# Performance work log

Hardware: AMD Instinct MI355X
Metric: run time of the kernel (lower is better)

Reference implementation:

```python
import jax, jax.numpy as jnp
import numpy as np
import math

B, D, C_LEN, Q_LEN = 32, 128, 1024, 256
NEG = -1e30

def setup_inputs() -> dict:
    key = jax.random.key(0)
    ks = jax.random.split(key, 8)
    bound = 1.0 / math.sqrt(D)
    return {
        "C": jax.random.normal(ks[0], (B, D, C_LEN), jnp.float32),
        "Q": jax.random.normal(ks[1], (B, D, Q_LEN), jnp.float32),
        "c_mask": jnp.ones((B, C_LEN), jnp.float32),
        "q_mask": jnp.ones((B, Q_LEN), jnp.float32),
        "W0": jax.random.uniform(ks[2], (3 * D,), jnp.float32, -bound, bound),
        # depthwise conv1d: in=4D groups=4D kernel=5 -> weight (4D, 1, 5)
        "dw_w": jax.random.normal(ks[3], (4 * D, 1, 5), jnp.float32) * math.sqrt(2.0 / 5),
        "dw_b": jnp.zeros((4 * D,), jnp.float32),
        # pointwise conv1d: 4D -> D, kernel 1
        "pw_w": jax.random.normal(ks[4], (D, 4 * D, 1), jnp.float32) * math.sqrt(2.0 / (4 * D)),
        "pw_b": jnp.zeros((D,), jnp.float32),
    }

def reference(C, Q, c_mask, q_mask, W0, dw_w, dw_b, pw_w, pw_b):
    d = W0.shape[0] // 3
    C_t = jnp.swapaxes(C, 1, 2)  # (B, c_len, d)
    Q_t = jnp.swapaxes(Q, 1, 2)  # (B, q_len, d)
    w1, w2, w3 = W0[:d], W0[d:2 * d], W0[2 * d:]
    # Trilinear similarity without materializing (B,c,q,3d):
    # S[b,i,j] = C_t[b,i].w1 + Q_t[b,j].w2 + sum_k C_t[b,i,k]*Q_t[b,j,k]*w3[k]
    S = (jnp.einsum('bik,bjk->bij', C_t * w3, Q_t)
         + (C_t @ w1)[:, :, None] + (Q_t @ w2)[:, None, :])  # (B, c_len, q_len)
    q_m = q_mask[:, None, :]
    c_m = c_mask[:, :, None]
    S_bar = jax.nn.softmax(S * q_m + NEG * (1.0 - q_m), axis=2)
    S_bbar = jax.nn.softmax(S * c_m + NEG * (1.0 - c_m), axis=1)
    A = jnp.einsum('bij,bjk->bik', S_bar, Q_t)                       # (B, c_len, d)
    # bmm(S_bar, S_bbar^T) @ C_t  ==  S_bar @ (S_bbar^T @ C_t)
    Bm = jnp.einsum('bij,bjk->bik', S_bar, jnp.einsum('bij,bik->bjk', S_bbar, C_t))
    out = jnp.concatenate([C_t, A, C_t * A, C_t * Bm], axis=2)       # (B, c_len, 4d)
    x = jnp.swapaxes(out, 1, 2)  # (B, 4d, c_len)
    # depthwise separable conv (eval mode: dropout is identity)
    x = jax.lax.conv_general_dilated(x, dw_w, (1,), [(2, 2)],
                                     dimension_numbers=('NCH', 'OIH', 'NCH'),
                                     feature_group_count=x.shape[1]) + dw_b[None, :, None]
    x = jax.lax.conv_general_dilated(x, pw_w, (1,), [(0, 0)],
                                     dimension_numbers=('NCH', 'OIH', 'NCH')) + pw_b[None, :, None]
    return x  # (B, d, c_len)
```

## Files before the change

kernel.cpp:

```cpp
#include <hip/hip_runtime.h>
#include <math.h>

#define NB 32
#define ND 128
#define NC 1024
#define NQ 256
#define NEGV (-1e30f)

typedef __attribute__((ext_vector_type(8))) __bf16 bf16x8;
typedef __attribute__((ext_vector_type(4))) float f32x4;
typedef __attribute__((ext_vector_type(8))) unsigned short u16x8;
typedef __attribute__((ext_vector_type(4))) unsigned short u16x4;

__device__ inline unsigned short f2bf(float f) {
  unsigned u = __builtin_bit_cast(unsigned, f);
  u += 0x7FFFu + ((u >> 16) & 1u);
  return (unsigned short)(u >> 16);
}
__device__ inline float bf2f(unsigned short u) {
  return __builtin_bit_cast(float, (unsigned)u << 16);
}

__global__ __launch_bounds__(256) void k_pwcvt(const float* __restrict__ pwW, unsigned short* __restrict__ pwB16) {
  int idx = blockIdx.x * 256 + threadIdx.x;
  const float4* src = (const float4*)pwW;
  float4 v0 = src[idx * 2], v1 = src[idx * 2 + 1];
  u16x8 o;
  o[0] = f2bf(v0.x); o[1] = f2bf(v0.y); o[2] = f2bf(v0.z); o[3] = f2bf(v0.w);
  o[4] = f2bf(v1.x); o[5] = f2bf(v1.y); o[6] = f2bf(v1.z); o[7] = f2bf(v1.w);
  ((u16x8*)pwB16)[idx] = o;
}

__global__ __launch_bounds__(256) void k_qprep(const float* __restrict__ Q, const float* __restrict__ W0,
                                               unsigned short* __restrict__ qSwz, unsigned short* __restrict__ qT,
                                               float* __restrict__ qb) {
  __shared__ unsigned short T2[128 * 66];
  __shared__ float w2L[128];
  __shared__ float qbP[4][64];
  int b = blockIdx.y, jc = blockIdx.x, j0 = jc * 64, t = threadIdx.x;
  if (t < 128) w2L[t] = W0[ND + t];
  int d = t >> 1, half = t & 1;
  const float* src = Q + ((size_t)b * ND + d) * NQ + j0 + half * 32;
  unsigned short* qdst = qSwz + ((size_t)b * ND + d) * NQ + jc * 64;
  #pragma unroll
  for (int q = 0; q < 4; ++q) {
    float4 v0 = ((const float4*)src)[q * 2];
    float4 v1 = ((const float4*)src)[q * 2 + 1];
    u16x8 o;
    o[0] = f2bf(v0.x); o[1] = f2bf(v0.y); o[2] = f2bf(v0.z); o[3] = f2bf(v0.w);
    o[4] = f2bf(v1.x); o[5] = f2bf(v1.y); o[6] = f2bf(v1.z); o[7] = f2bf(v1.w);
    *(u16x8*)&T2[d * 66 + half * 32 + q * 8] = o;
    int g = half * 4 + q;
    *(u16x8*)&qdst[(g ^ (d & 7)) * 8] = o;
  }
  __syncthreads();
  {
    int jj = t & 63, dq = t >> 6;
    float s = 0.f;
    #pragma unroll 8
    for (int k = 0; k < 32; ++k) {
      int dd = dq * 32 + k;
      s += bf2f(T2[dd * 66 + jj]) * w2L[dd];
    }
    qbP[dq][jj] = s;
  }
  __syncthreads();
  if (t < 64)
    qb[b * NQ + j0 + t] = qbP[0][t] + qbP[1][t] + qbP[2][t] + qbP[3][t];
  {
    int jj = t >> 2, p = t & 3;
    unsigned short* dst = qT + ((size_t)b * NQ + j0 + jj) * ND;
    #pragma unroll
    for (int q = 0; q < 4; ++q) {
      int g = p * 4 + q;
      u16x8 o;
      #pragma unroll
      for (int e = 0; e < 8; ++e) o[e] = T2[(g * 8 + e) * 66 + jj];
      int sg = (g & 8) | ((g & 7) ^ (jj & 7));
      *(u16x8*)&dst[sg * 8] = o;
    }
  }
}

__global__ __launch_bounds__(256) void k_cprep(const float* __restrict__ C, const float* __restrict__ W0,
                                               unsigned short* __restrict__ cw3T, unsigned short* __restrict__ cSwz,
                                               float* __restrict__ cb) {
  __shared__ unsigned short T2[128 * 66];
  __shared__ float w1L[128], w3L[128];
  __shared__ float cbP[4][64];
  int b = blockIdx.y, i0 = blockIdx.x * 64, t = threadIdx.x;
  if (t < 128) { w1L[t] = W0[t]; w3L[t] = W0[2 * ND + t]; }
  int k = t >> 1, half = t & 1;
  const float* src = C + ((size_t)b * ND + k) * NC + i0 + half * 32;
  unsigned short* cdst = cSwz + ((size_t)b * ND + k) * NC + blockIdx.x * 64;
  #pragma unroll
  for (int q = 0; q < 4; ++q) {
    float4 v0 = ((const float4*)src)[q * 2];
    float4 v1 = ((const float4*)src)[q * 2 + 1];
    u16x8 o;
    o[0] = f2bf(v0.x); o[1] = f2bf(v0.y); o[2] = f2bf(v0.z); o[3] = f2bf(v0.w);
    o[4] = f2bf(v1.x); o[5] = f2bf(v1.y); o[6] = f2bf(v1.z); o[7] = f2bf(v1.w);
    *(u16x8*)&T2[k * 66 + half * 32 + q * 8] = o;
    int g = half * 4 + q;
    *(u16x8*)&cdst[(g ^ (k & 7)) * 8] = o;
  }
  __syncthreads();
  {
    int ii = t & 63, kq = t >> 6;
    float s = 0.f;
    #pragma unroll 8
    for (int kk = 0; kk < 32; ++kk) {
      int dd = kq * 32 + kk;
      s += bf2f(T2[dd * 66 + ii]) * w1L[dd];
    }
    cbP[kq][ii] = s;
  }
  __syncthreads();
  if (t < 64)
    cb[b * NC + i0 + t] = cbP[0][t] + cbP[1][t] + cbP[2][t] + cbP[3][t];
  {
    int ii = t >> 2, p = t & 3;
    unsigned short* dst = cw3T + ((size_t)b * NC + i0 + ii) * ND;
    #pragma unroll
    for (int q = 0; q < 4; ++q) {
      int g = p * 4 + q;
      u16x8 o;
      #pragma unroll
      for (int e = 0; e < 8; ++e)
        o[e] = f2bf(bf2f(T2[(g * 8 + e) * 66 + ii]) * w3L[g * 8 + e]);
      int sg = (g & 8) | ((g & 7) ^ (ii & 7));
      *(u16x8*)&dst[sg * 8] = o;
    }
  }
}

__global__ __launch_bounds__(256) void k_stats(const unsigned short* __restrict__ cw3T,
                                               const unsigned short* __restrict__ qT,
                                               const float* __restrict__ cb, const float* __restrict__ qb,
                                               const float* __restrict__ q_mask, const float* __restrict__ c_mask,
                                               float* __restrict__ rowmax, float* __restrict__ rowsum,
                                               float* __restrict__ colPm, float* __restrict__ colPs) {
  __shared__ float rmP[64][4], rsP[64][4];
  __shared__ float cbL[64], cmL[64], qbL[256], qmL[256];
  int b = blockIdx.y, i0 = blockIdx.x * 64;
  int t = threadIdx.x, w = t >> 6, l = t & 63, h = l >> 4, lr = l & 15;
  int wj = w * 64;
  if (t < 64) { cbL[t] = cb[b * NC + i0 + t]; cmL[t] = c_mask[b * NC + i0 + t]; }
  qbL[t] = qb[b * NQ + t];
  qmL[t] = q_mask[b * NQ + t];
  const unsigned short* Arow = cw3T + ((size_t)b * NC + i0) * ND;
  const unsigned short* Brow = qT + (size_t)b * NQ * ND;
  f32x4 acc[4][4] = {};
  #pragma unroll
  for (int ks = 0; ks < 4; ++ks) {
    int g = ks * 4 + h;
    int off = ((g & 8) | ((g & 7) ^ (lr & 7))) * 8;
    bf16x8 a[4], bq[4];
    #pragma unroll
    for (int mi = 0; mi < 4; ++mi)
      a[mi] = *(const bf16x8*)&Arow[(size_t)(mi * 16 + lr) * ND + off];
    #pragma unroll
    for (int nf = 0; nf < 4; ++nf)
      bq[nf] = *(const bf16x8*)&Brow[(size_t)(wj + nf * 16 + lr) * ND + off];
    #pragma unroll
    for (int mi = 0; mi < 4; ++mi)
      #pragma unroll
      for (int nf = 0; nf < 4; ++nf)
        acc[mi][nf] = __builtin_amdgcn_mfma_f32_16x16x32_bf16(a[mi], bq[nf], acc[mi][nf], 0, 0, 0);
  }
  __syncthreads();
  float qbv[4], qmv[4];
  #pragma unroll
  for (int nf = 0; nf < 4; ++nf) {
    int j = wj + nf * 16 + lr;
    qbv[nf] = qbL[j]; qmv[nf] = qmL[j];
  }
  float rmv[4][4], rsv[4][4];
  #pragma unroll
  for (int mi = 0; mi < 4; ++mi)
    #pragma unroll
    for (int r = 0; r < 4; ++r) { rmv[mi][r] = -3.0e38f; rsv[mi][r] = 0.f; }
  #pragma unroll
  for (int mi = 0; mi < 4; ++mi) {
    #pragma unroll
    for (int r = 0; r < 4; ++r) {
      int row = mi * 16 + h * 4 + r;
      float cbr = cbL[row];
      #pragma unroll
      for (int nf = 0; nf < 4; ++nf) {
        float sv = acc[mi][nf][r] + cbr + qbv[nf];
        acc[mi][nf][r] = sv;
        float vq = sv * qmv[nf] + NEGV * (1.f - qmv[nf]);
        float mn = fmaxf(rmv[mi][r], vq);
        rsv[mi][r] = rsv[mi][r] * __expf(rmv[mi][r] - mn) + __expf(vq - mn);
        rmv[mi][r] = mn;
      }
    }
  }
  #pragma unroll
  for (int off = 1; off < 16; off <<= 1) {
    #pragma unroll
    for (int mi = 0; mi < 4; ++mi)
      #pragma unroll
      for (int r = 0; r < 4; ++r) {
        float mo = __shfl_xor(rmv[mi][r], off);
        float so = __shfl_xor(rsv[mi][r], off);
        float mn = fmaxf(rmv[mi][r], mo);
        rsv[mi][r] = rsv[mi][r] * __expf(rmv[mi][r] - mn) + so * __expf(mo - mn);
        rmv[mi][r] = mn;
      }
  }
  if (lr == 0) {
    #pragma unroll
    for (int mi = 0; mi < 4; ++mi)
      #pragma unroll
      for (int r = 0; r < 4; ++r) {
        rmP[mi * 16 + h * 4 + r][w] = rmv[mi][r];
        rsP[mi * 16 + h * 4 + r][w] = rsv[mi][r];
      }
  }
  float pm[4], ps[4];
  #pragma unroll
  for (int nf = 0; nf < 4; ++nf) { pm[nf] = -3.0e38f; ps[nf] = 0.f; }
  #pragma unroll
  for (int mi = 0; mi < 4; ++mi)
    #pragma unroll
    for (int r = 0; r < 4; ++r) {
      int row = mi * 16 + h * 4 + r;
      float cm = cmL[row];
      float cbias = NEGV * (1.f - cm);
      #pragma unroll
      for (int nf = 0; nf < 4; ++nf) {
        float v = acc[mi][nf][r] * cm + cbias;
        float mn = fmaxf(pm[nf], v);
        ps[nf] = ps[nf] * __expf(pm[nf] - mn) + __expf(v - mn);
        pm[nf] = mn;
      }
    }
  #pragma unroll
  for (int off = 16; off < 64; off <<= 1) {
    #pragma unroll
    for (int nf = 0; nf < 4; ++nf) {
      float mo = __shfl_xor(pm[nf], off);
      float so = __shfl_xor(ps[nf], off);
      float mn = fmaxf(pm[nf], mo);
      ps[nf] = ps[nf] * __expf(pm[nf] - mn) + so * __expf(mo - mn);
      pm[nf] = mn;
    }
  }
  if (h == 0) {
    #pragma unroll
    for (int nf = 0; nf < 4; ++nf) {
      int j = wj + nf * 16 + lr;
      colPm[((size_t)blockIdx.x * NB + b) * NQ + j] = pm[nf];
      colPs[((size_t)blockIdx.x * NB + b) * NQ + j] = ps[nf];
    }
  }
  __syncthreads();
  if (t < 64) {
    float m = rmP[t][0], s = rsP[t][0];
    #pragma unroll
    for (int k = 1; k < 4; ++k) {
      float mo = rmP[t][k], so = rsP[t][k];
      float mn = fmaxf(m, mo);
      s = s * __expf(m - mn) + so * __expf(mo - mn);
      m = mn;
    }
    rowmax[b * NC + i0 + t] = m;
    rowsum[b * NC + i0 + t] = s;
  }
}

__global__ __launch_bounds__(256) void k4f(const unsigned short* __restrict__ cw3T,
                                           const unsigned short* __restrict__ qT,
                                           const unsigned short* __restrict__ cSwz,
                                           const float* __restrict__ cb, const float* __restrict__ qb,
                                           const float* __restrict__ c_mask,
                                           const float* __restrict__ colPm, const float* __restrict__ colPs,
                                           float* __restrict__ partial) {
  __shared__ unsigned short Pt[32 * 72];
  __shared__ float cmxL[32], cinvL[32], qbL2[32], cbL[64], cmL[64];
  int b = blockIdx.y;
  int jt = blockIdx.x & 7, split = blockIdx.x >> 3;
  int j0 = jt * 32;
  int t = threadIdx.x, w = t >> 6, l = t & 63, h = l >> 4, lr = l & 15;
  if (t < 32) {
    float m = -3.0e38f, s = 0.f;
    #pragma unroll
    for (int tl = 0; tl < 16; ++tl) {
      float mo = colPm[((size_t)tl * NB + b) * NQ + j0 + t];
      float so = colPs[((size_t)tl * NB + b) * NQ + j0 + t];
      float mn = fmaxf(m, mo);
      s = s * __expf(m - mn) + so * __expf(mo - mn);
      m = mn;
    }
    cmxL[t] = m;
    cinvL[t] = 1.0f / s;
    qbL2[t] = qb[b * NQ + j0 + t];
  }
  const unsigned short* Ab = cw3T + (size_t)b * NC * ND;
  const unsigned short* Bb = qT + ((size_t)b * NQ + j0) * ND;
  const unsigned short* Cb2 = cSwz + (size_t)b * ND * NC;
  f32x4 accI[2][2] = {};
  for (int ic8 = 0; ic8 < 8; ++ic8) {
    int ic = split * 512 + ic8 * 64;
    if (t < 64) { cbL[t] = cb[b * NC + ic + t]; cmL[t] = c_mask[b * NC + ic + t]; }
    __syncthreads();
    f32x4 sA[2] = {};
    #pragma unroll
    for (int ks = 0; ks < 4; ++ks) {
      int g = ks * 4 + h;
      int off = ((g & 8) | ((g & 7) ^ (lr & 7))) * 8;
      bf16x8 av = *(const bf16x8*)&Ab[(size_t)(ic + w * 16 + lr) * ND + off];
      #pragma unroll
      for (int jf = 0; jf < 2; ++jf) {
        bf16x8 bv = *(const bf16x8*)&Bb[(size_t)(jf * 16 + lr) * ND + off];
        sA[jf] = __builtin_amdgcn_mfma_f32_16x16x32_bf16(av, bv, sA[jf], 0, 0, 0);
      }
    }
    #pragma unroll
    for (int jf = 0; jf < 2; ++jf)
      #pragma unroll
      for (int r = 0; r < 4; ++r) {
        int i_ = w * 16 + h * 4 + r;
        int j_ = jf * 16 + lr;
        float sfull = sA[jf][r] + cbL[i_] + qbL2[j_];
        float cm = cmL[i_];
        float vc = sfull * cm + NEGV * (1.f - cm);
        float p = __expf(vc - cmxL[j_]) * cinvL[j_];
        Pt[j_ * 72 + (((i_ >> 3) ^ (j_ & 7)) << 3) + (i_ & 7)] = f2bf(p);
      }
    __syncthreads();
    #pragma unroll
    for (int ks = 0; ks < 2; ++ks) {
      bf16x8 aC[2], bP[2];
      #pragma unroll
      for (int mf = 0; mf < 2; ++mf) {
        int d = w * 32 + mf * 16 + lr;
        aC[mf] = *(const bf16x8*)&Cb2[(size_t)d * NC + ic + (((ks * 4 + h) ^ (lr & 7)) * 8)];
      }
      #pragma unroll
      for (int jf = 0; jf < 2; ++jf) {
        int j_ = jf * 16 + lr;
        bP[jf] = *(const bf16x8*)&Pt[j_ * 72 + (((ks * 4 + h) ^ (j_ & 7)) * 8)];
      }
      #pragma unroll
      for (int mf = 0; mf < 2; ++mf)
        #pragma unroll
        for (int jf = 0; jf < 2; ++jf)
          accI[mf][jf] = __builtin_amdgcn_mfma_f32_16x16x32_bf16(aC[mf], bP[jf], accI[mf][jf], 0, 0, 0);
    }
  }
  float* pout = partial + ((size_t)(split * NB + b) * ND) * NQ;
  #pragma unroll
  for (int mf = 0; mf < 2; ++mf)
    #pragma unroll
    for (int jf = 0; jf < 2; ++jf)
      #pragma unroll
      for (int r = 0; r < 4; ++r) {
        int d = w * 32 + mf * 16 + h * 4 + r;
        int j = j0 + jf * 16 + lr;
        pout[(size_t)d * NQ + j] = accI[mf][jf][r];
      }
}

__global__ __launch_bounds__(256) void k4c2(const float* __restrict__ partial,
                                            unsigned short* __restrict__ iSwz) {
  int idx = blockIdx.x * 256 + threadIdx.x;
  const size_t n = (size_t)NB * ND * NQ / 4;
  const float4* p = (const float4*)partial;
  float4 a = p[idx], b4 = p[n + idx];
  u16x4 o;
  o[0] = f2bf(a.x + b4.x);
  o[1] = f2bf(a.y + b4.y);
  o[2] = f2bf(a.z + b4.z);
  o[3] = f2bf(a.w + b4.w);
  int lin = idx * 4;
  int j = lin & 255, dd = (lin >> 8) & 127, bb = lin >> 15;
  int g = (j >> 3) & 7, e0 = j & 7;
  int outoff = ((bb * 128 + dd) << 8) + (j & 192) + ((g ^ (dd & 7)) << 3) + e0;
  *(u16x4*)&iSwz[outoff] = o;
}

__global__ __launch_bounds__(256) void k5f(const unsigned short* __restrict__ cw3T,
                                           const unsigned short* __restrict__ qT,
                                           const unsigned short* __restrict__ qSwz,
                                           const unsigned short* __restrict__ iSwz,
                                           const float* __restrict__ C,
                                           const float* __restrict__ cb, const float* __restrict__ qb,
                                           const float* __restrict__ q_mask,
                                           const float* __restrict__ rowmax, const float* __restrict__ rowsum,
                                           unsigned short* __restrict__ xB) {
  extern __shared__ char sm[];
  unsigned short* cwA = (unsigned short*)sm;
  unsigned short* Pl = (unsigned short*)(sm + 8192);
  float* As = (float*)sm;
  float* Bs = (float*)(sm + 17024);
  __shared__ float rmL[32], riL[32], cbI[32], qbL[256], qmL[256];
  int b = blockIdx.y, i0 = blockIdx.x * 32;
  int t = threadIdx.x, w = t >> 6, l = t & 63, h = l >> 4, lr = l & 15;
  {
    const unsigned short* src = cw3T + ((size_t)b * NC + i0) * ND;
    #pragma unroll
    for (int k = 0; k < 2; ++k) {
      int u = t + k * 256;
      *(u16x8*)&cwA[u * 8] = *(const u16x8*)(src + u * 8);
    }
  }
  if (t < 32) {
    rmL[t] = rowmax[b * NC + i0 + t];
    riL[t] = 1.0f / rowsum[b * NC + i0 + t];
    cbI[t] = cb[b * NC + i0 + t];
  }
  qbL[t] = qb[b * NQ + t];
  qmL[t] = q_mask[b * NQ + t];
  __syncthreads();

  const unsigned short* qTb = qT + (size_t)b * NQ * ND;
  const unsigned short* qSb = qSwz + (size_t)b * ND * NQ;
  const unsigned short* iSb = iSwz + (size_t)b * ND * NQ;
  f32x4 accA[2][2] = {};
  f32x4 accB[2][2] = {};

  for (int jc = 0; jc < 4; ++jc) {
    int j0 = jc * 64;
    f32x4 sA[2] = {};
    #pragma unroll
    for (int ks = 0; ks < 4; ++ks) {
      int g = ks * 4 + h;
      int off = ((g & 8) | ((g & 7) ^ (lr & 7))) * 8;
      bf16x8 bv = *(const bf16x8*)&qTb[(size_t)(j0 + w * 16 + lr) * ND + off];
      #pragma unroll
      for (int mi = 0; mi < 2; ++mi) {
        bf16x8 av = *(const bf16x8*)&cwA[(mi * 16 + lr) * 128 + off];
        sA[mi] = __builtin_amdgcn_mfma_f32_16x16x32_bf16(av, bv, sA[mi], 0, 0, 0);
      }
    }
    #pragma unroll
    for (int mi = 0; mi < 2; ++mi)
      #pragma unroll
      for (int r = 0; r < 4; ++r) {
        int i_ = mi * 16 + h * 4 + r;
        int j_ = w * 16 + lr;
        float sfull = sA[mi][r] + cbI[i_] + qbL[j0 + j_];
        float qm = qmL[j0 + j_];
        float vq = sfull * qm + NEGV * (1.f - qm);
        float p = __expf(vq - rmL[i_]) * riL[i_];
        Pl[i_ * 72 + (((j_ >> 3) ^ (i_ & 7)) << 3) + (j_ & 7)] = f2bf(p);
      }
    __syncthreads();
    #pragma unroll
    for (int ks = 0; ks < 2; ++ks) {
      bf16x8 aP[2], bQ[2], bI[2];
      #pragma unroll
      for (int mi = 0; mi < 2; ++mi) {
        int i = mi * 16 + lr;
        int slot = (ks * 4 + h) ^ (i & 7);
        aP[mi] = *(const bf16x8*)&Pl[i * 72 + slot * 8];
      }
      #pragma unroll
      for (int nd = 0; nd < 2; ++nd) {
        int d = w * 32 + nd * 16 + lr;
        int slot = (ks * 4 + h) ^ (d & 7);
        bQ[nd] = *(const bf16x8*)&qSb[(size_t)d * NQ + j0 + slot * 8];
        bI[nd] = *(const bf16x8*)&iSb[(size_t)d * NQ + j0 + slot * 8];
      }
      #pragma unroll
      for (int mi = 0; mi < 2; ++mi)
        #pragma unroll
        for (int nd = 0; nd < 2; ++nd) {
          accA[mi][nd] = __builtin_amdgcn_mfma_f32_16x16x32_bf16(aP[mi], bQ[nd], accA[mi][nd], 0, 0, 0);
          accB[mi][nd] = __builtin_amdgcn_mfma_f32_16x16x32_bf16(aP[mi], bI[nd], accB[mi][nd], 0, 0, 0);
        }
    }
    __syncthreads();
  }
  #pragma unroll
  for (int mi = 0; mi < 2; ++mi)
    #pragma unroll
    for (int nd = 0; nd < 2; ++nd) {
      int d = w * 32 + nd * 16 + lr;
      #pragma unroll
      for (int r = 0; r < 4; ++r) {
        int i = mi * 16 + h * 4 + r;
        As[i * 133 + d] = accA[mi][nd][r];
        Bs[i * 133 + d] = accB[mi][nd][r];
      }
    }
  __syncthreads();
  {
    int i4 = (t & 7) * 4, db = t >> 3;
    const float* Cb = C + (size_t)b * ND * NC;
    unsigned short* xb = xB + (size_t)b * 4 * ND * NC;
    #pragma unroll
    for (int p = 0; p < 4; ++p) {
      int d = db + p * 32;
      float4 c4 = *(const float4*)&Cb[(size_t)d * NC + i0 + i4];
      float4 a4, b4;
      a4.x = As[(i4 + 0) * 133 + d]; a4.y = As[(i4 + 1) * 133 + d];
      a4.z = As[(i4 + 2) * 133 + d]; a4.w = As[(i4 + 3) * 133 + d];
      b4.x = Bs[(i4 + 0) * 133 + d]; b4.y = Bs[(i4 + 1) * 133 + d];
      b4.z = Bs[(i4 + 2) * 133 + d]; b4.w = Bs[(i4 + 3) * 133 + d];
      u16x4 o0, o1, o2, o3;
      o0[0] = f2bf(c4.x); o0[1] = f2bf(c4.y); o0[2] = f2bf(c4.z); o0[3] = f2bf(c4.w);
      o1[0] = f2bf(a4.x); o1[1] = f2bf(a4.y); o1[2] = f2bf(a4.z); o1[3] = f2bf(a4.w);
      o2[0] = f2bf(c4.x * a4.x); o2[1] = f2bf(c4.y * a4.y); o2[2] = f2bf(c4.z * a4.z); o2[3] = f2bf(c4.w * a4.w);
      o3[0] = f2bf(c4.x * b4.x); o3[1] = f2bf(c4.y * b4.y); o3[2] = f2bf(c4.z * b4.z); o3[3] = f2bf(c4.w * b4.w);
      *(u16x4*)&xb[(size_t)(0 * ND + d) * NC + i0 + i4] = o0;
      *(u16x4*)&xb[(size_t)(1 * ND + d) * NC + i0 + i4] = o1;
      *(u16x4*)&xb[(size_t)(2 * ND + d) * NC + i0 + i4] = o2;
      *(u16x4*)&xb[(size_t)(3 * ND + d) * NC + i0 + i4] = o3;
    }
  }
}

__global__ __launch_bounds__(256) void k6_mfma(const unsigned short* __restrict__ x,
                                               const float* __restrict__ dwW, const float* __restrict__ dwB,
                                               const unsigned short* __restrict__ pwB16,
                                               const float* __restrict__ pwB, float* __restrict__ out) {
  extern __shared__ char sm6[];
  unsigned short* xs = (unsigned short*)sm6;
  unsigned short* x1s = (unsigned short*)(sm6 + 7168);
  unsigned short* pws = (unsigned short*)(sm6 + 11776);
  int b = blockIdx.y, l0 = blockIdx.x * 32;
  int t = threadIdx.x, w = t >> 6, l = t & 63, h = l >> 4, lr = l & 15;
  const unsigned short* xb = x + (size_t)b * 4 * ND * NC;
  f32x4 acc[2][2] = {};
  int cgw = t & 63, lb = w * 8;

  for (int ch = 0; ch < 8; ++ch) {
    int cg0 = ch * 64;
    __syncthreads();
    #pragma unroll
    for (int k = 0; k < 2; ++k) {
      int id2 = t + k * 256;
      if (id2 < 384) {
        int row = id2 / 6, seg = id2 % 6;
        int gl = l0 - 8 + seg * 8;
        u16x8 v = {};
        if ((unsigned)gl <= 1016u)
          v = *(const u16x8*)(xb + (size_t)(cg0 + row) * NC + gl);
        *(u16x8*)&xs[row * 56 + seg * 8] = v;
      }
    }
    #pragma unroll
    for (int k = 0; k < 4; ++k) {
      int id2 = t + k * 256;
      int o = id2 >> 3, s8 = id2 & 7;
      *(u16x8*)&pws[o * 72 + s8 * 8] = *(const u16x8*)(pwB16 + (size_t)o * 512 + cg0 + s8 * 8);
    }
    __syncthreads();
    {
      int gch = cg0 + cgw;
      float bias = dwB[gch];
      float dwv[5];
      #pragma unroll
      for (int tp = 0; tp < 5; ++tp) dwv[tp] = dwW[gch * 5 + tp];
      float f[24];
      #pragma unroll
      for (int s = 0; s < 3; ++s) {
        u16x8 v = *(const u16x8*)&xs[cgw * 56 + lb + s * 8];
        #pragma unroll
        for (int e = 0; e < 8; ++e) f[s * 8 + e] = bf2f(v[e]);
      }
      #pragma unroll
      for (int e = 0; e < 8; ++e) {
        float a = bias;
        #pragma unroll
        for (int tp = 0; tp < 5; ++tp)
          a = fmaf(f[e + 6 + tp], dwv[tp], a);
        x1s[(lb + e) * 72 + cgw] = f2bf(a);
      }
    }
    __syncthreads();
    #pragma unroll
    for (int ks = 0; ks < 2; ++ks) {
      bf16x8 aW[2], bX[2];
      #pragma unroll
      for (int mi = 0; mi < 2; ++mi) {
        int o = w * 32 + mi * 16 + lr;
        aW[mi] = *(const bf16x8*)&pws[o * 72 + ks * 32 + h * 8];
      }
      #pragma unroll
      for (int nf = 0; nf < 2; ++nf) {
        int ll = nf * 16 + lr;
        bX[nf] = *(const bf16x8*)&x1s[ll * 72 + ks * 32 + h * 8];
      }
      #pragma unroll
      for (int mi = 0; mi < 2; ++mi)
        #pragma unroll
        for (int nf = 0; nf < 2; ++nf)
          acc[mi][nf] = __builtin_amdgcn_mfma_f32_16x16x32_bf16(aW[mi], bX[nf], acc[mi][nf], 0, 0, 0);
    }
  }
  #pragma unroll
  for (int mi = 0; mi < 2; ++mi) {
    #pragma unroll
    for (int r = 0; r < 4; ++r) {
      int o = w * 32 + mi * 16 + h * 4 + r;
      float bv = pwB[o];
      #pragma unroll
      for (int nf = 0; nf < 2; ++nf)
        out[((size_t)b * ND + o) * NC + l0 + nf * 16 + lr] = acc[mi][nf][r] + bv;
    }
  }
}

extern "C" void kernel_launch(void* const* d_in, const int* in_sizes, int n_in,
                              void* d_out, int out_size, void* d_ws, size_t ws_size,
                              hipStream_t stream) {
  const float* C = (const float*)d_in[0];
  const float* Q = (const float*)d_in[1];
  const float* c_mask = (const float*)d_in[2];
  const float* q_mask = (const float*)d_in[3];
  const float* W0 = (const float*)d_in[4];
  const float* dwW = (const float*)d_in[5];
  const float* dwB = (const float*)d_in[6];
  const float* pwW = (const float*)d_in[7];
  const float* pwB = (const float*)d_in[8];
  float* out = (float*)d_out;
  float* ws = (float*)d_ws;

  float* rowmax = ws;
  float* rowsum = rowmax + NB * NC;
  float* colmax = rowsum + NB * NC;
  float* colsum = colmax + NB * NQ;
  float* cb = colsum + NB * NQ;
  float* qb = cb + NB * NC;
  float* colPm = qb + NB * NQ;
  float* colPs = colPm + 16 * NB * NQ;
  unsigned short* qSwz = (unsigned short*)(colPs + 16 * NB * NQ);
  unsigned short* qT = qSwz + (size_t)NB * ND * NQ;
  unsigned short* iSwz = qT + (size_t)NB * NQ * ND;
  unsigned short* cw3T = iSwz + (size_t)NB * ND * NQ;
  unsigned short* cSwz = cw3T + (size_t)NB * NC * ND;
  unsigned short* pwB16 = cSwz + (size_t)NB * ND * NC;
  float* partial = (float*)(pwB16 + ND * 512);
  unsigned short* xB = (unsigned short*)(partial + 2 * (size_t)NB * ND * NQ);

  k_pwcvt<<<dim3(32), 256, 0, stream>>>(pwW, pwB16);
  k_qprep<<<dim3(4, NB), 256, 0, stream>>>(Q, W0, qSwz, qT, qb);
  k_cprep<<<dim3(16, NB), 256, 0, stream>>>(C, W0, cw3T, cSwz, cb);
  k_stats<<<dim3(16, NB), 256, 0, stream>>>(cw3T, qT, cb, qb, q_mask, c_mask, rowmax, rowsum, colPm, colPs);
  k4f<<<dim3(16, NB), 256, 0, stream>>>(cw3T, qT, cSwz, cb, qb, c_mask, colPm, colPs, partial);
  k4c2<<<dim3(NB * ND * NQ / 4 / 256), 256, 0, stream>>>(partial, iSwz);
  k5f<<<dim3(NC / 32, NB), 256, 34048, stream>>>(cw3T, qT, qSwz, iSwz, C, cb, qb, q_mask, rowmax, rowsum, xB);
  k6_mfma<<<dim3(NC / 32, NB), 256, 30208, stream>>>(xB, dwW, dwB, pwB16, pwB, out);
}
```

Baseline: 117.5 us.

## Merge prep kernels into one launch and fold partial-sum reduction into k5f

Combines the three preprocessing kernels (C prep, Q prep, pointwise-weight conversion) into a single launch that dispatches on block index. It also removes the k4c2 kernel: k5f now reads the two fp32 split-K partials directly, sums them and converts to bf16 on the fly. This cuts three kernel launches and the intermediate write and read of iSwz. In exchange, each of the 32 k5f blocks per batch re-reads the fp32 partials (four times the bytes of the bf16 array) and repeats the add and convert.

Result: slower. 139.4 us (+18.6%).

```diff
diff --git a/kernel.cpp b/kernel.cpp
--- a/kernel.cpp
+++ b/kernel.cpp
@@ -21,116 +21,114 @@
   return __builtin_bit_cast(float, (unsigned)u << 16);
 }
 
-__global__ __launch_bounds__(256) void k_pwcvt(const float* __restrict__ pwW, unsigned short* __restrict__ pwB16) {
-  int idx = blockIdx.x * 256 + threadIdx.x;
-  const float4* src = (const float4*)pwW;
-  float4 v0 = src[idx * 2], v1 = src[idx * 2 + 1];
-  u16x8 o;
-  o[0] = f2bf(v0.x); o[1] = f2bf(v0.y); o[2] = f2bf(v0.z); o[3] = f2bf(v0.w);
-  o[4] = f2bf(v1.x); o[5] = f2bf(v1.y); o[6] = f2bf(v1.z); o[7] = f2bf(v1.w);
-  ((u16x8*)pwB16)[idx] = o;
-}
-
-__global__ __launch_bounds__(256) void k_qprep(const float* __restrict__ Q, const float* __restrict__ W0,
-                                               unsigned short* __restrict__ qSwz, unsigned short* __restrict__ qT,
-                                               float* __restrict__ qb) {
+__global__ __launch_bounds__(256) void k_prep(const float* __restrict__ C, const float* __restrict__ Q,
+                                              const float* __restrict__ pwW, const float* __restrict__ W0,
+                                              unsigned short* __restrict__ cw3T, unsigned short* __restrict__ cSwz,
+                                              float* __restrict__ cb,
+                                              unsigned short* __restrict__ qSwz, unsigned short* __restrict__ qT,
+                                              float* __restrict__ qb,
+                                              unsigned short* __restrict__ pwB16) {
   __shared__ unsigned short T2[128 * 66];
-  __shared__ float w2L[128];
-  __shared__ float qbP[4][64];
-  int b = blockIdx.y, jc = blockIdx.x, j0 = jc * 64, t = threadIdx.x;
-  if (t < 128) w2L[t] = W0[ND + t];
-  int d = t >> 1, half = t & 1;
-  const float* src = Q + ((size_t)b * ND + d) * NQ + j0 + half * 32;
-  unsigned short* qdst = qSwz + ((size_t)b * ND + d) * NQ + jc * 64;
-  #pragma unroll
-  for (int q = 0; q < 4; ++q) {
-    float4 v0 = ((const float4*)src)[q * 2];
-    float4 v1 = ((const float4*)src)[q * 2 + 1];
+  __shared__ float wA[128], wB[128];
+  __shared__ float redP[4][64];
+  int bid = blockIdx.x, t = threadIdx.x;
+  if (bid < 512) {
+    int b = bid >> 4, tile = bid & 15, i0 = tile * 64;
+    if (t < 128) { wA[t] = W0[t]; wB[t] = W0[2 * ND + t]; }
+    int k = t >> 1, half = t & 1;
+    const float* src = C + ((size_t)b * ND + k) * NC + i0 + half * 32;
+    unsigned short* cdst = cSwz + ((size_t)b * ND + k) * NC + tile * 64;
+    #pragma unroll
+    for (int q = 0; q < 4; ++q) {
+      float4 v0 = ((const float4*)src)[q * 2];
+      float4 v1 = ((const float4*)src)[q * 2 + 1];
+      u16x8 o;
+      o[0] = f2bf(v0.x); o[1] = f2bf(v0.y); o[2] = f2bf(v0.z); o[3] = f2bf(v0.w);
+      o[4] = f2bf(v1.x); o[5] = f2bf(v1.y); o[6] = f2bf(v1.z); o[7] = f2bf(v1.w);
+      *(u16x8*)&T2[k * 66 + half * 32 + q * 8] = o;
+      int g = half * 4 + q;
+      *(u16x8*)&cdst[(g ^ (k & 7)) * 8] = o;
+    }
+    __syncthreads();
+    {
+      int ii = t & 63, kq = t >> 6;
+      float s = 0.f;
+      #pragma unroll 8
+      for (int kk = 0; kk < 32; ++kk) {
+        int dd = kq * 32 + kk;
+        s += bf2f(T2[dd * 66 + ii]) * wA[dd];
+      }
+      redP[kq][ii] = s;
+    }
+    __syncthreads();
+    if (t < 64)
+      cb[b * NC + i0 + t] = redP[0][t] + redP[1][t] + redP[2][t] + redP[3][t];
+    {
+      int ii = t >> 2, p = t & 3;
+      unsigned short* dst = cw3T + ((size_t)b * NC + i0 + ii) * ND;
+      #pragma unroll
+      for (int q = 0; q < 4; ++q) {
+        int g = p * 4 + q;
+        u16x8 o;
+        #pragma unroll
+        for (int e = 0; e < 8; ++e)
+          o[e] = f2bf(bf2f(T2[(g * 8 + e) * 66 + ii]) * wB[g * 8 + e]);
+        int sg = (g & 8) | ((g & 7) ^ (ii & 7));
+        *(u16x8*)&dst[sg * 8] = o;
+      }
+    }
+  } else if (bid < 640) {
+    int r = bid - 512, b = r >> 2, jc = r & 3, j0 = jc * 64;
+    if (t < 128) wA[t] = W0[ND + t];
+    int d = t >> 1, half = t & 1;
+    const float* src = Q + ((size_t)b * ND + d) * NQ + j0 + half * 32;
+    unsigned short* qdst = qSwz + ((size_t)b * ND + d) * NQ + jc * 64;
+    #pragma unroll
+    for (int q = 0; q < 4; ++q) {
+      float4 v0 = ((const float4*)src)[q * 2];
+      float4 v1 = ((const float4*)src)[q * 2 + 1];
+      u16x8 o;
+      o[0] = f2bf(v0.x); o[1] = f2bf(v0.y); o[2] = f2bf(v0.z); o[3] = f2bf(v0.w);
+      o[4] = f2bf(v1.x); o[5] = f2bf(v1.y); o[6] = f2bf(v1.z); o[7] = f2bf(v1.w);
+      *(u16x8*)&T2[d * 66 + half * 32 + q * 8] = o;
+      int g = half * 4 + q;
+      *(u16x8*)&qdst[(g ^ (d & 7)) * 8] = o;
+    }
+    __syncthreads();
+    {
+      int jj = t & 63, dq = t >> 6;
+      float s = 0.f;
+      #pragma unroll 8
+      for (int k = 0; k < 32; ++k) {
+        int dd = dq * 32 + k;
+        s += bf2f(T2[dd * 66 + jj]) * wA[dd];
+      }
+      redP[dq][jj] = s;
+    }
+    __syncthreads();
+    if (t < 64)
+      qb[b * NQ + j0 + t] = redP[0][t] + redP[1][t] + redP[2][t] + redP[3][t];
+    {
+      int jj = t >> 2, p = t & 3;
+      unsigned short* dst = qT + ((size_t)b * NQ + j0 + jj) * ND;
+      #pragma unroll
+      for (int q = 0; q < 4; ++q) {
+        int g = p * 4 + q;
+        u16x8 o;
+        #pragma unroll
+        for (int e = 0; e < 8; ++e) o[e] = T2[(g * 8 + e) * 66 + jj];
+        int sg = (g & 8) | ((g & 7) ^ (jj & 7));
+        *(u16x8*)&dst[sg * 8] = o;
+      }
+    }
+  } else {
+    int idx = (bid - 640) * 256 + t;
+    const float4* src = (const float4*)pwW;
+    float4 v0 = src[idx * 2], v1 = src[idx * 2 + 1];
     u16x8 o;
     o[0] = f2bf(v0.x); o[1] = f2bf(v0.y); o[2] = f2bf(v0.z); o[3] = f2bf(v0.w);
     o[4] = f2bf(v1.x); o[5] = f2bf(v1.y); o[6] = f2bf(v1.z); o[7] = f2bf(v1.w);
-    *(u16x8*)&T2[d * 66 + half * 32 + q * 8] = o;
-    int g = half * 4 + q;
-    *(u16x8*)&qdst[(g ^ (d & 7)) * 8] = o;
-  }
-  __syncthreads();
-  {
-    int jj = t & 63, dq = t >> 6;
-    float s = 0.f;
-    #pragma unroll 8
-    for (int k = 0; k < 32; ++k) {
-      int dd = dq * 32 + k;
-      s += bf2f(T2[dd * 66 + jj]) * w2L[dd];
-    }
-    qbP[dq][jj] = s;
-  }
-  __syncthreads();
-  if (t < 64)
-    qb[b * NQ + j0 + t] = qbP[0][t] + qbP[1][t] + qbP[2][t] + qbP[3][t];
-  {
-    int jj = t >> 2, p = t & 3;
-    unsigned short* dst = qT + ((size_t)b * NQ + j0 + jj) * ND;
-    #pragma unroll
-    for (int q = 0; q < 4; ++q) {
-      int g = p * 4 + q;
-      u16x8 o;
-      #pragma unroll
-      for (int e = 0; e < 8; ++e) o[e] = T2[(g * 8 + e) * 66 + jj];
-      int sg = (g & 8) | ((g & 7) ^ (jj & 7));
-      *(u16x8*)&dst[sg * 8] = o;
-    }
-  }
-}
-
-__global__ __launch_bounds__(256) void k_cprep(const float* __restrict__ C, const float* __restrict__ W0,
-                                               unsigned short* __restrict__ cw3T, unsigned short* __restrict__ cSwz,
-                                               float* __restrict__ cb) {
-  __shared__ unsigned short T2[128 * 66];
-  __shared__ float w1L[128], w3L[128];
-  __shared__ float cbP[4][64];
-  int b = blockIdx.y, i0 = blockIdx.x * 64, t = threadIdx.x;
-  if (t < 128) { w1L[t] = W0[t]; w3L[t] = W0[2 * ND + t]; }
-  int k = t >> 1, half = t & 1;
-  const float* src = C + ((size_t)b * ND + k) * NC + i0 + half * 32;
-  unsigned short* cdst = cSwz + ((size_t)b * ND + k) * NC + blockIdx.x * 64;
-  #pragma unroll
-  for (int q = 0; q < 4; ++q) {
-    float4 v0 = ((const float4*)src)[q * 2];
-    float4 v1 = ((const float4*)src)[q * 2 + 1];
-    u16x8 o;
-    o[0] = f2bf(v0.x); o[1] = f2bf(v0.y); o[2] = f2bf(v0.z); o[3] = f2bf(v0.w);
-    o[4] = f2bf(v1.x); o[5] = f2bf(v1.y); o[6] = f2bf(v1.z); o[7] = f2bf(v1.w);
-    *(u16x8*)&T2[k * 66 + half * 32 + q * 8] = o;
-    int g = half * 4 + q;
-    *(u16x8*)&cdst[(g ^ (k & 7)) * 8] = o;
-  }
-  __syncthreads();
-  {
-    int ii = t & 63, kq = t >> 6;
-    float s = 0.f;
-    #pragma unroll 8
-    for (int kk = 0; kk < 32; ++kk) {
-      int dd = kq * 32 + kk;
-      s += bf2f(T2[dd * 66 + ii]) * w1L[dd];
-    }
-    cbP[kq][ii] = s;
-  }
-  __syncthreads();
-  if (t < 64)
-    cb[b * NC + i0 + t] = cbP[0][t] + cbP[1][t] + cbP[2][t] + cbP[3][t];
-  {
-    int ii = t >> 2, p = t & 3;
-    unsigned short* dst = cw3T + ((size_t)b * NC + i0 + ii) * ND;
-    #pragma unroll
-    for (int q = 0; q < 4; ++q) {
-      int g = p * 4 + q;
-      u16x8 o;
-      #pragma unroll
-      for (int e = 0; e < 8; ++e)
-        o[e] = f2bf(bf2f(T2[(g * 8 + e) * 66 + ii]) * w3L[g * 8 + e]);
-      int sg = (g & 8) | ((g & 7) ^ (ii & 7));
-      *(u16x8*)&dst[sg * 8] = o;
-    }
+    ((u16x8*)pwB16)[idx] = o;
   }
 }
 
@@ -364,28 +362,10 @@
       }
 }
 
-__global__ __launch_bounds__(256) void k4c2(const float* __restrict__ partial,
-                                            unsigned short* __restrict__ iSwz) {
-  int idx = blockIdx.x * 256 + threadIdx.x;
-  const size_t n = (size_t)NB * ND * NQ / 4;
-  const float4* p = (const float4*)partial;
-  float4 a = p[idx], b4 = p[n + idx];
-  u16x4 o;
-  o[0] = f2bf(a.x + b4.x);
-  o[1] = f2bf(a.y + b4.y);
-  o[2] = f2bf(a.z + b4.z);
-  o[3] = f2bf(a.w + b4.w);
-  int lin = idx * 4;
-  int j = lin & 255, dd = (lin >> 8) & 127, bb = lin >> 15;
-  int g = (j >> 3) & 7, e0 = j & 7;
-  int outoff = ((bb * 128 + dd) << 8) + (j & 192) + ((g ^ (dd & 7)) << 3) + e0;
-  *(u16x4*)&iSwz[outoff] = o;
-}
-
 __global__ __launch_bounds__(256) void k5f(const unsigned short* __restrict__ cw3T,
                                            const unsigned short* __restrict__ qT,
                                            const unsigned short* __restrict__ qSwz,
-                                           const unsigned short* __restrict__ iSwz,
+                                           const float* __restrict__ partial,
                                            const float* __restrict__ C,
                                            const float* __restrict__ cb, const float* __restrict__ qb,
                                            const float* __restrict__ q_mask,
@@ -418,7 +398,8 @@
 
   const unsigned short* qTb = qT + (size_t)b * NQ * ND;
   const unsigned short* qSb = qSwz + (size_t)b * ND * NQ;
-  const unsigned short* iSb = iSwz + (size_t)b * ND * NQ;
+  const float* iP0 = partial + (size_t)b * ND * NQ;
+  const float* iP1 = partial + ((size_t)(NB + b)) * ND * NQ;
   f32x4 accA[2][2] = {};
   f32x4 accB[2][2] = {};
 
@@ -451,6 +432,7 @@
     __syncthreads();
     #pragma unroll
     for (int ks = 0; ks < 2; ++ks) {
+      int jbase = j0 + (ks * 4 + h) * 8;
       bf16x8 aP[2], bQ[2], bI[2];
       #pragma unroll
       for (int mi = 0; mi < 2; ++mi) {
@@ -463,7 +445,16 @@
         int d = w * 32 + nd * 16 + lr;
         int slot = (ks * 4 + h) ^ (d & 7);
         bQ[nd] = *(const bf16x8*)&qSb[(size_t)d * NQ + j0 + slot * 8];
-        bI[nd] = *(const bf16x8*)&iSb[(size_t)d * NQ + j0 + slot * 8];
+        float4 p0a = *(const float4*)&iP0[(size_t)d * NQ + jbase];
+        float4 p0b = *(const float4*)&iP0[(size_t)d * NQ + jbase + 4];
+        float4 p1a = *(const float4*)&iP1[(size_t)d * NQ + jbase];
+        float4 p1b = *(const float4*)&iP1[(size_t)d * NQ + jbase + 4];
+        u16x8 bi;
+        bi[0] = f2bf(p0a.x + p1a.x); bi[1] = f2bf(p0a.y + p1a.y);
+        bi[2] = f2bf(p0a.z + p1a.z); bi[3] = f2bf(p0a.w + p1a.w);
+        bi[4] = f2bf(p0b.x + p1b.x); bi[5] = f2bf(p0b.y + p1b.y);
+        bi[6] = f2bf(p0b.z + p1b.z); bi[7] = f2bf(p0b.w + p1b.w);
+        bI[nd] = __builtin_bit_cast(bf16x8, bi);
       }
       #pragma unroll
       for (int mi = 0; mi < 2; ++mi)
@@ -638,12 +629,9 @@
   float* partial = (float*)(pwB16 + ND * 512);
   unsigned short* xB = (unsigned short*)(partial + 2 * (size_t)NB * ND * NQ);
 
-  k_pwcvt<<<dim3(32), 256, 0, stream>>>(pwW, pwB16);
-  k_qprep<<<dim3(4, NB), 256, 0, stream>>>(Q, W0, qSwz, qT, qb);
-  k_cprep<<<dim3(16, NB), 256, 0, stream>>>(C, W0, cw3T, cSwz, cb);
+  k_prep<<<dim3(672), 256, 0, stream>>>(C, Q, pwW, W0, cw3T, cSwz, cb, qSwz, qT, qb, pwB16);
   k_stats<<<dim3(16, NB), 256, 0, stream>>>(cw3T, qT, cb, qb, q_mask, c_mask, rowmax, rowsum, colPm, colPs);
   k4f<<<dim3(16, NB), 256, 0, stream>>>(cw3T, qT, cSwz, cb, qb, c_mask, colPm, colPs, partial);
-  k4c2<<<dim3(NB * ND * NQ / 4 / 256), 256, 0, stream>>>(partial, iSwz);
-  k5f<<<dim3(NC / 32, NB), 256, 34048, stream>>>(cw3T, qT, qSwz, iSwz, C, cb, qb, q_mask, rowmax, rowsum, xB);
+  k5f<<<dim3(NC / 32, NB), 256, 34048, stream>>>(cw3T, qT, qSwz, partial, C, cb, qb, q_mask, rowmax, rowsum, xB);
   k6_mfma<<<dim3(NC / 32, NB), 256, 30208, stream>>>(xB, dwW, dwB, pwB16, pwB, out);
 }
```
